# Optimization experiments

Measured on AMD Instinct MI355X. Metric: run time of the kernel, lower is better.

The kernel has to match this reference:

```python
import jax, jax.numpy as jnp
import numpy as np

HEADS = 8
EPS = 1e-5

def _conv2d(x, w, b):
    # x: (b,c,h,w), w: (out_c,in_c,3,3), padding=1 (SAME)
    y = jax.lax.conv_general_dilated(x, w, (1, 1), ((1, 1), (1, 1)),
                                     dimension_numbers=('NCHW', 'OIHW', 'NCHW'))
    return y + b[None, :, None, None]

def _mcl(x, cw, cb, pw):
    # MultichannelLinear: conv then per-channel pointwise matmul over the h (feature) dim
    y = _conv2d(x, cw, cb)                      # (b,c,in_f,w)
    return jnp.einsum('bchw,cfh->bcfw', y, pw)  # (b,c,out_f,w)

def _ln(x, g, b):
    # MultichannelLayerNorm over the feature (h) axis with per-channel affine
    mu = x.mean(axis=2, keepdims=True)
    var = x.var(axis=2, keepdims=True)
    xn = (x - mu) * jax.lax.rsqrt(var + EPS)
    return xn * g[None, :, :, None] + b[None, :, :, None]

def _rope(t):
    # lucidrains RotaryEmbedding.rotate_queries_or_keys, interleaved pairs; t: (...,w,d)
    d = t.shape[-1]
    w = t.shape[-2]
    inv = 1.0 / (10000.0 ** (jnp.arange(0, d, 2, dtype=jnp.float32) / d))
    ang = jnp.arange(w, dtype=jnp.float32)[:, None] * inv[None, :]   # (w, d/2)
    cos = jnp.repeat(jnp.cos(ang), 2, axis=-1)
    sin = jnp.repeat(jnp.sin(ang), 2, axis=-1)
    t2 = t.reshape(t.shape[:-1] + (d // 2, 2))
    rot = jnp.stack([-t2[..., 1], t2[..., 0]], axis=-1).reshape(t.shape)
    return t * cos + rot * sin

def _split_heads(y, nh):
    b, c, f, w = y.shape
    return y.transpose(0, 1, 3, 2).reshape(b, c, w, nh, f // nh).transpose(0, 1, 3, 2, 4)  # (b,c,nh,w,dh)

def _forward(x, embed_cw, embed_cb, embed_pw, norm1_g, norm1_b,
             q_cw, q_cb, q_pw, k_cw, k_cb, k_pw, v_cw, v_cb, v_pw,
             o_cw, o_cb, o_pw, norm2_g, norm2_b,
             ffn1_cw, ffn1_cb, ffn1_pw, ffn2_cw, ffn2_cb, ffn2_pw):
    b, c_in, hdim, w = x.shape
    h0 = _mcl(x, embed_cw, embed_cb, embed_pw)          # (b,c,feat,w)
    # --- multichannel multihead attention with inline RoPE ---
    xn = _ln(h0, norm1_g, norm1_b)
    q = _rope(_split_heads(_mcl(xn, q_cw, q_cb, q_pw), HEADS))   # (b,c,nh,w,dh)
    k = _rope(_split_heads(_mcl(xn, k_cw, k_cb, k_pw), HEADS))
    v = _split_heads(_mcl(xn, v_cw, v_cb, v_pw), HEADS)
    qk = jnp.einsum('bchqd,bchkd->bchqk', q, k) / jnp.sqrt(jnp.float32(hdim))  # scale by sqrt(h), per source
    a = jnp.einsum('bchqk,bchkd->bchqd', jax.nn.softmax(qk, axis=-1), v)
    bb, cc, nh, ww, dh = a.shape
    a = a.transpose(0, 1, 3, 2, 4).reshape(bb, cc, ww, nh * dh).transpose(0, 1, 3, 2)  # (b,c,feat,w)
    z = _mcl(a, o_cw, o_cb, o_pw)
    h = h0 + z
    # --- squared-ReLU FFN ---
    y = _mcl(_ln(h, norm2_g, norm2_b), ffn1_cw, ffn1_cb, ffn1_pw)
    y = jnp.maximum(y, 0.0) ** 2
    z = _mcl(y, ffn2_cw, ffn2_cb, ffn2_pw)
    h = h + z
    return jnp.concatenate([x, h], axis=1)  # (b, c_in+c_out, feat, w)

def setup_inputs() -> dict:
    key = jax.random.key(0)
    ks = jax.random.split(key, 32)
    C_IN, C, F, W, B, EXP = 8, 4, 1024, 512, 4, 4

    def p(k, shape, fan):
        return jax.random.normal(k, shape, dtype=jnp.float32) * (1.0 / np.sqrt(fan))

    inp = {
        'x': jax.random.normal(ks[0], (B, C_IN, F, W), dtype=jnp.float32),
        'embed_cw': p(ks[1], (C, C_IN, 3, 3), C_IN * 9), 'embed_cb': p(ks[2], (C,), C_IN * 9),
        'embed_pw': p(ks[3], (C, F, F), F),
        'norm1_g': jnp.ones((C, F), jnp.float32), 'norm1_b': jnp.zeros((C, F), jnp.float32),
        'q_cw': p(ks[4], (C, C, 3, 3), C * 9), 'q_cb': p(ks[5], (C,), C * 9), 'q_pw': p(ks[6], (C, F, F), F),
        'k_cw': p(ks[7], (C, C, 3, 3), C * 9), 'k_cb': p(ks[8], (C,), C * 9), 'k_pw': p(ks[9], (C, F, F), F),
        'v_cw': p(ks[10], (C, C, 3, 3), C * 9), 'v_cb': p(ks[11], (C,), C * 9), 'v_pw': p(ks[12], (C, F, F), F),
        'o_cw': p(ks[13], (C, C, 3, 3), C * 9), 'o_cb': p(ks[14], (C,), C * 9), 'o_pw': p(ks[15], (C, F, F), F),
        'norm2_g': jnp.ones((C, F), jnp.float32), 'norm2_b': jnp.zeros((C, F), jnp.float32),
        'ffn1_cw': p(ks[16], (C, C, 3, 3), C * 9), 'ffn1_cb': p(ks[17], (C,), C * 9),
        'ffn1_pw': p(ks[18], (C, F * EXP, F), F),
        'ffn2_cw': p(ks[19], (C, C, 3, 3), C * 9), 'ffn2_cb': p(ks[20], (C,), C * 9),
        'ffn2_pw': p(ks[21], (C, F, F * EXP), F * EXP),
    }
    return inp

def reference(x, embed_cw, embed_cb, embed_pw, norm1_g, norm1_b,
              q_cw, q_cb, q_pw, k_cw, k_cb, k_pw, v_cw, v_cb, v_pw,
              o_cw, o_cb, o_pw, norm2_g, norm2_b,
              ffn1_cw, ffn1_cb, ffn1_pw, ffn2_cw, ffn2_cb, ffn2_pw):
    return _forward(x, embed_cw, embed_cb, embed_pw, norm1_g, norm1_b,
                    q_cw, q_cb, q_pw, k_cw, k_cb, k_pw, v_cw, v_cb, v_pw,
                    o_cw, o_cb, o_pw, norm2_g, norm2_b,
                    ffn1_cw, ffn1_cb, ffn1_pw, ffn2_cw, ffn2_cb, ffn2_pw)
```

## Files before the change

### kernel.cpp

```cpp
#include <hip/hip_runtime.h>

typedef __attribute__((ext_vector_type(8))) short short8;
typedef __attribute__((ext_vector_type(4))) float f32x4;
typedef unsigned int uint;
typedef unsigned short ushort;

#define PLF 524288

__device__ __forceinline__ ushort f2bf(float f) {
  uint u = __float_as_uint(f);
  u += 0x7FFF + ((u >> 16) & 1);
  return (ushort)(u >> 16);
}
__device__ __forceinline__ float bf2f(ushort h) {
  return __uint_as_float(((uint)h) << 16);
}
__device__ __forceinline__ int swzf(int r) { return ((r & 3) ^ ((r >> 2) & 3)); }

#define GLOAD16(gp, lp)                                          \
  __builtin_amdgcn_global_load_lds(                              \
      (const __attribute__((address_space(1))) void*)(gp),       \
      (__attribute__((address_space(3))) void*)(lp), 16, 0, 0)

template <int CDT, int BETA, int RELU2, int MFAST, int BCVT, int ROPE>
__global__ __launch_bounds__(256) void mm_kernel(
    const void* __restrict__ Av, const void* __restrict__ Bv, void* __restrict__ Cv,
    int K, int lda, int ldb, int ldc,
    int aDiv, int aMod, long long aS1, long long aS2,
    int bDiv, int bMod, long long bS1, long long bS2,
    int cDiv, int cMod, long long cS1, long long cS2, float alpha)
{
  __shared__ char lds[49152];
  const int nx = gridDim.x, ny = gridDim.y;
  const int nwg = nx * ny * (int)gridDim.z;
  const int o = ((int)blockIdx.z * ny + blockIdx.y) * nx + blockIdx.x;
  const int qd = nwg >> 3, rm = nwg & 7, xcd = o & 7, rot = o >> 3;
  const int wflat = (xcd < rm ? xcd * (qd + 1) : rm * (qd + 1) + (xcd - rm) * qd) + rot;
  int bx, by, bz;
  if (MFAST) { by = wflat % ny; int t2 = wflat / ny; bx = t2 % nx; bz = t2 / nx; }
  else       { bx = wflat % nx; int t2 = wflat / nx; by = t2 % ny; bz = t2 / ny; }
  const int tid = threadIdx.x;
  const long long aOff = (long long)(bz / aDiv) * aS1 + (long long)(bz % aMod) * aS2;
  const long long bOff = (long long)(bz / bDiv) * bS1 + (long long)(bz % bMod) * bS2;
  const long long cOff = (long long)(bz / cDiv) * cS1 + (long long)(bz % cMod) * cS2;
  const int m0 = by * 128, n0 = bx * 128;
  const int lane = tid & 63, wid = tid >> 6;
  const int MOFF = (wid >> 1) * 64, NOFF = (wid & 1) * 64;
  const int u = lane & 15, g = lane >> 4;
  const int sr0 = tid >> 2, sslot = tid & 3;
  const ushort* Ap = (const ushort*)Av + aOff;
  const ushort* Bp = (const ushort*)Bv + bOff;
  const float*  Bf = (const float*)Bv + bOff;

#define STAGE(buf, kt)                                                         \
  {                                                                            \
    _Pragma("unroll")                                                          \
    for (int half = 0; half < 2; ++half) {                                     \
      const int r = sr0 + 64 * half;                                           \
      const int ss = sslot ^ swzf(r);                                          \
      GLOAD16(Ap + (long long)(m0 + r) * lda + (kt) + ss * 8,                  \
              &lds[(buf) * 16384] + wid * 1024 + half * 4096);                 \
      if (BCVT == 0) {                                                         \
        GLOAD16(Bp + (long long)(n0 + r) * ldb + (kt) + ss * 8,                \
                &lds[(buf) * 16384 + 8192] + wid * 1024 + half * 4096);        \
      } else {                                                                 \
        const float* srcB = Bf + (long long)(n0 + r) * ldb + (kt) + ss * 8;    \
        float4 x0 = *(const float4*)srcB;                                      \
        float4 x1 = *(const float4*)(srcB + 4);                                \
        short8 h;                                                              \
        h[0] = (short)f2bf(x0.x); h[1] = (short)f2bf(x0.y);                    \
        h[2] = (short)f2bf(x0.z); h[3] = (short)f2bf(x0.w);                    \
        h[4] = (short)f2bf(x1.x); h[5] = (short)f2bf(x1.y);                    \
        h[6] = (short)f2bf(x1.z); h[7] = (short)f2bf(x1.w);                    \
        *(short8*)(&lds[(buf) * 16384 + 8192] + r * 64 + sslot * 16) = h;      \
      }                                                                        \
    }                                                                          \
  }

  f32x4 acc[4][4];
#pragma unroll
  for (int i = 0; i < 4; ++i)
#pragma unroll
    for (int j = 0; j < 4; ++j) acc[i][j] = (f32x4){0.f, 0.f, 0.f, 0.f};

  const int T = K >> 5;
  STAGE(0, 0);
  if (T > 1) STAGE(1, 32);
  int rb = 0, sb = 2;
  for (int t = 0; t < T; ++t) {
    if (BCVT == 0) {
      if (t + 1 < T) { asm volatile("s_waitcnt vmcnt(4)" ::: "memory"); }
      else           { asm volatile("s_waitcnt vmcnt(0)" ::: "memory"); }
    } else {
      asm volatile("s_waitcnt vmcnt(0) lgkmcnt(0)" ::: "memory");
    }
    __builtin_amdgcn_s_barrier();
    __builtin_amdgcn_sched_barrier(0);
    asm volatile("" ::: "memory");
    if (t + 2 < T) STAGE(sb, (t + 2) * 32);
    const char* Abuf = &lds[rb * 16384];
    const char* Bbuf = &lds[rb * 16384 + 8192];
    short8 af[4], bfr[4];
#pragma unroll
    for (int mi = 0; mi < 4; ++mi) {
      const int r = MOFF + mi * 16 + u;
      af[mi] = *(const short8*)(Abuf + r * 64 + ((g ^ swzf(r)) * 16));
    }
#pragma unroll
    for (int ni = 0; ni < 4; ++ni) {
      const int r = NOFF + ni * 16 + u;
      bfr[ni] = *(const short8*)(Bbuf + r * 64 + ((g ^ swzf(r)) * 16));
    }
#pragma unroll
    for (int mi = 0; mi < 4; ++mi)
#pragma unroll
      for (int ni = 0; ni < 4; ++ni)
        acc[mi][ni] = __builtin_amdgcn_mfma_f32_16x16x32_bf16(af[mi], bfr[ni], acc[mi][ni], 0, 0, 0);
    rb = (rb == 2) ? 0 : rb + 1;
    sb = (sb == 2) ? 0 : sb + 1;
  }
#undef STAGE

#pragma unroll
  for (int mi = 0; mi < 4; ++mi)
#pragma unroll
    for (int ni = 0; ni < 4; ++ni)
#pragma unroll
      for (int q = 0; q < 4; ++q) {
        const int row = m0 + MOFF + mi * 16 + g * 4 + q;
        const int col = n0 + NOFF + ni * 16 + u;
        float v = acc[mi][ni][q] * alpha;
        if (CDT == 0) {
          float* cp = (float*)Cv + cOff + (long long)row * ldc + col;
          if (BETA) v += *cp;
          *cp = v;
        } else {
          if (ROPE) {
            const int j = (col & 127) >> 1;
            const float infr = __expf((float)j * (-9.210340371976184f / 64.f));
            float sn, cs;
            __sincosf((float)row * infr, &sn, &cs);
            const float part = __shfl_xor(v, 1);
            v = (col & 1) ? fmaf(part, sn, v * cs) : fmaf(-part, sn, v * cs);
          }
          if (RELU2) { v = fmaxf(v, 0.f); v = v * v; }
          ((ushort*)Cv)[cOff + (long long)row * ldc + col] = f2bf(v);
        }
      }
}

__global__ __launch_bounds__(256) void fattn_kernel(
    const ushort* __restrict__ Qg, const ushort* __restrict__ Kg,
    const ushort* __restrict__ Vg, ushort* __restrict__ Og)
{
  __shared__ char lds[73728];
  const int hb = blockIdx.y, pl = hb >> 3, h = hb & 7;
  const int q0 = blockIdx.x * 64;
  const int tid = threadIdx.x, lane = tid & 63, wv = tid >> 6;
  const int u = lane & 15, g = lane >> 4;
  const ushort* Qh = Qg + (size_t)pl * PLF + h * 128;
  const ushort* Kh = Kg + (size_t)pl * PLF + h * 128;
  const ushort* Vh = Vg + (size_t)pl * PLF + (size_t)(h * 128) * 512;
  ushort* Oh = Og + (size_t)pl * PLF + h * 128;

  short8 qf[4];
  const int qrow = q0 + wv * 16 + u;
#pragma unroll
  for (int dc = 0; dc < 4; ++dc)
    qf[dc] = *(const short8*)(Qh + (size_t)qrow * 1024 + dc * 32 + g * 8);

#define STAGE_KV(buf, kt)                                                     \
  {                                                                           \
    _Pragma("unroll")                                                         \
    for (int it = 0; it < 4; ++it) {                                          \
      const int off = tid * 16 + it * 4096;                                   \
      const int krow = off >> 8, kslot = (off >> 4) & 15;                     \
      GLOAD16(Kh + (size_t)((kt) * 64 + krow) * 1024 +                        \
                  ((kslot ^ ((krow & 7) << 1)) * 8),                          \
              &lds[(buf) * 16384] + off);                                     \
      const int vrow = off >> 7, vslot = (off >> 4) & 7;                      \
      GLOAD16(Vh + (size_t)vrow * 512 + (kt) * 64 + ((vslot ^ (vrow & 7)) * 8), \
              &lds[32768 + (buf) * 16384] + off);                             \
    }                                                                         \
  }

  f32x4 oacc[8];
#pragma unroll
  for (int i = 0; i < 8; ++i) oacc[i] = (f32x4){0.f, 0.f, 0.f, 0.f};
  float m_run = -3.0e38f, l_run = 0.f;

  STAGE_KV(0, 0);
  asm volatile("s_waitcnt vmcnt(0)" ::: "memory");
  __syncthreads();
  int cur = 0;
  for (int kt = 0; kt < 8; ++kt) {
    if (kt + 1 < 8) STAGE_KV(cur ^ 1, kt + 1);
    f32x4 sacc[4];
#pragma unroll
    for (int kn = 0; kn < 4; ++kn) sacc[kn] = (f32x4){0.f, 0.f, 0.f, 0.f};
#pragma unroll
    for (int kn = 0; kn < 4; ++kn) {
      const int r = kn * 16 + u;
      const char* kb = &lds[cur * 16384] + r * 256;
#pragma unroll
      for (int dc = 0; dc < 4; ++dc) {
        short8 kf = *(const short8*)(kb + (((dc * 4 + g) ^ ((u & 7) << 1)) * 16));
        sacc[kn] = __builtin_amdgcn_mfma_f32_16x16x32_bf16(kf, qf[dc], sacc[kn], 0, 0, 0);
      }
    }
    float pm = -3.0e38f;
#pragma unroll
    for (int kn = 0; kn < 4; ++kn)
#pragma unroll
      for (int r = 0; r < 4; ++r) {
        sacc[kn][r] *= 0.03125f;
        pm = fmaxf(pm, sacc[kn][r]);
      }
    pm = fmaxf(pm, __shfl_xor(pm, 16));
    pm = fmaxf(pm, __shfl_xor(pm, 32));
    const float m_new = fmaxf(m_run, pm);
    const float es = __expf(m_run - m_new);
    float psum = 0.f;
    uint pw[4][2];
#pragma unroll
    for (int kn = 0; kn < 4; ++kn) {
      float p0 = __expf(sacc[kn][0] - m_new);
      float p1 = __expf(sacc[kn][1] - m_new);
      float p2 = __expf(sacc[kn][2] - m_new);
      float p3 = __expf(sacc[kn][3] - m_new);
      psum += (p0 + p1) + (p2 + p3);
      pw[kn][0] = (uint)f2bf(p0) | ((uint)f2bf(p1) << 16);
      pw[kn][1] = (uint)f2bf(p2) | ((uint)f2bf(p3) << 16);
    }
    psum += __shfl_xor(psum, 16);
    psum += __shfl_xor(psum, 32);
    l_run = l_run * es + psum;
    m_run = m_new;
    char* pb = &lds[65536 + wv * 2048] + u * 128 + (g & 1) * 8;
#pragma unroll
    for (int kn = 0; kn < 4; ++kn)
      *(uint2*)(pb + (((2 * kn + (g >> 1)) ^ (u & 7)) * 16)) =
          make_uint2(pw[kn][0], pw[kn][1]);
    float es_o[4];
#pragma unroll
    for (int r = 0; r < 4; ++r) es_o[r] = __shfl(es, g * 4 + r);
#pragma unroll
    for (int nd = 0; nd < 8; ++nd)
#pragma unroll
      for (int r = 0; r < 4; ++r) oacc[nd][r] *= es_o[r];
    const char* prd = &lds[65536 + wv * 2048] + u * 128;
    short8 pf[2];
#pragma unroll
    for (int kc = 0; kc < 2; ++kc)
      pf[kc] = *(const short8*)(prd + (((kc * 4 + g) ^ (u & 7)) * 16));
#pragma unroll
    for (int nd = 0; nd < 8; ++nd) {
      const int vr = nd * 16 + u;
      const char* vb = &lds[32768 + cur * 16384] + vr * 128;
#pragma unroll
      for (int kc = 0; kc < 2; ++kc) {
        short8 vf = *(const short8*)(vb + (((kc * 4 + g) ^ (u & 7)) * 16));
        oacc[nd] = __builtin_amdgcn_mfma_f32_16x16x32_bf16(pf[kc], vf, oacc[nd], 0, 0, 0);
      }
    }
    asm volatile("s_waitcnt vmcnt(0)" ::: "memory");
    __syncthreads();
    cur ^= 1;
  }
#undef STAGE_KV
  const float inv_l = 1.f / l_run;
  float inv_o[4];
#pragma unroll
  for (int r = 0; r < 4; ++r) inv_o[r] = __shfl(inv_l, g * 4 + r);
#pragma unroll
  for (int nd = 0; nd < 8; ++nd)
#pragma unroll
    for (int r = 0; r < 4; ++r) {
      const int row = q0 + wv * 16 + g * 4 + r;
      Oh[(size_t)row * 1024 + nd * 16 + u] = f2bf(oacc[nd][r] * inv_o[r]);
    }
}

__global__ __launch_bounds__(256) void cvt_kernel(
    const float4* __restrict__ s, short8* __restrict__ d)
{
  const int i = blockIdx.x * 256 + threadIdx.x;
  const float4 a = s[2 * i], b = s[2 * i + 1];
  short8 h;
  h[0] = (short)f2bf(a.x); h[1] = (short)f2bf(a.y);
  h[2] = (short)f2bf(a.z); h[3] = (short)f2bf(a.w);
  h[4] = (short)f2bf(b.x); h[5] = (short)f2bf(b.y);
  h[6] = (short)f2bf(b.z); h[7] = (short)f2bf(b.w);
  d[i] = h;
}

template <int CIN>
__global__ __launch_bounds__(256) void conv4c_kernel(
    const ushort* __restrict__ in, const float* __restrict__ wt,
    const float* __restrict__ bias, ushort* __restrict__ outp, int log2F)
{
  const int idx = blockIdx.x * 256 + threadIdx.x;
  const int F8m = (1 << (log2F - 3)) - 1;
  const int f8 = idx & F8m;
  const int w = (idx >> (log2F - 3)) & 511;
  const int bb = idx >> (log2F + 6);
  const int f0 = f8 << 3;
  float acc[4][8];
#pragma unroll
  for (int co = 0; co < 4; ++co) {
    const float bv = bias[co];
#pragma unroll
    for (int j = 0; j < 8; ++j) acc[co][j] = bv;
  }
  const bool lok = f8 > 0, rok = f8 < F8m;
#pragma unroll
  for (int ci = 0; ci < CIN; ++ci) {
    const ushort* base = in + (((size_t)(bb * CIN + ci)) << (log2F + 9));
#pragma unroll
    for (int dxw = 0; dxw < 3; ++dxw) {
      const int w2 = w + dxw - 1;
      if (w2 < 0 || w2 > 511) continue;
      const ushort* rp = base + ((size_t)w2 << log2F) + f0;
      const short8 cen = *(const short8*)rp;
      float xv[10];
      xv[0] = lok ? bf2f(rp[-1]) : 0.f;
#pragma unroll
      for (int j = 0; j < 8; ++j) xv[j + 1] = bf2f((ushort)cen[j]);
      xv[9] = rok ? bf2f(rp[8]) : 0.f;
#pragma unroll
      for (int co = 0; co < 4; ++co) {
        const float* wp = wt + (co * CIN + ci) * 9;
        const float k0 = wp[dxw], k1 = wp[3 + dxw], k2 = wp[6 + dxw];
#pragma unroll
        for (int j = 0; j < 8; ++j)
          acc[co][j] += k0 * xv[j] + k1 * xv[j + 1] + k2 * xv[j + 2];
      }
    }
  }
#pragma unroll
  for (int co = 0; co < 4; ++co) {
    short8 o;
#pragma unroll
    for (int j = 0; j < 8; ++j) o[j] = (short)f2bf(acc[co][j]);
    *(short8*)(outp + (((size_t)(bb * 4 + co)) << (log2F + 9)) + ((size_t)w << log2F) + f0) = o;
  }
}

__global__ __launch_bounds__(256) void conv12c_kernel(
    const ushort* __restrict__ in,
    const float* __restrict__ wq, const float* __restrict__ wk, const float* __restrict__ wv,
    const float* __restrict__ bq, const float* __restrict__ bk, const float* __restrict__ bv,
    ushort* __restrict__ outp, int nPl)
{
  const int idx = blockIdx.x * 256 + threadIdx.x;
  const int f8 = idx & 127;
  const int w = (idx >> 7) & 511;
  const int bb = idx >> 16;
  const int f0 = f8 << 3;
  const float* wsel[3] = {wq, wk, wv};
  float acc[12][8];
#pragma unroll
  for (int co = 0; co < 4; ++co) {
    const float b0 = bq[co], b1 = bk[co], b2 = bv[co];
#pragma unroll
    for (int j = 0; j < 8; ++j) {
      acc[co][j] = b0; acc[4 + co][j] = b1; acc[8 + co][j] = b2;
    }
  }
  const bool lok = f8 > 0, rok = f8 < 127;
#pragma unroll
  for (int ci = 0; ci < 4; ++ci) {
    const ushort* base = in + (((size_t)(bb * 4 + ci)) << 19);
#pragma unroll
    for (int dxw = 0; dxw < 3; ++dxw) {
      const int w2 = w + dxw - 1;
      if (w2 < 0 || w2 > 511) continue;
      const ushort* rp = base + ((size_t)w2 << 10) + f0;
      const short8 cen = *(const short8*)rp;
      float xv[10];
      xv[0] = lok ? bf2f(rp[-1]) : 0.f;
#pragma unroll
      for (int j = 0; j < 8; ++j) xv[j + 1] = bf2f((ushort)cen[j]);
      xv[9] = rok ? bf2f(rp[8]) : 0.f;
#pragma unroll
      for (int pj = 0; pj < 3; ++pj)
#pragma unroll
        for (int co = 0; co < 4; ++co) {
          const float* wp = wsel[pj] + (co * 4 + ci) * 9;
          const float k0 = wp[dxw], k1 = wp[3 + dxw], k2 = wp[6 + dxw];
#pragma unroll
          for (int j = 0; j < 8; ++j)
            acc[pj * 4 + co][j] += k0 * xv[j] + k1 * xv[j + 1] + k2 * xv[j + 2];
        }
    }
  }
#pragma unroll
  for (int pj = 0; pj < 3; ++pj)
#pragma unroll
    for (int co = 0; co < 4; ++co) {
      short8 o;
#pragma unroll
      for (int j = 0; j < 8; ++j) o[j] = (short)f2bf(acc[pj * 4 + co][j]);
      *(short8*)(outp + (((size_t)(pj * nPl + bb * 4 + co)) << 19) +
                 ((size_t)w << 10) + f0) = o;
    }
}

__global__ __launch_bounds__(256) void ln_kernel(
    const float* __restrict__ H, const float* __restrict__ gam,
    const float* __restrict__ bet, ushort* __restrict__ XN)
{
  const int wid = threadIdx.x >> 6, lane = threadIdx.x & 63;
  const int row = blockIdx.x * 4 + wid;
  const int c = (row >> 9) & 3;
  const float* xp = H + (size_t)row * 1024;
  float4 v[4];
  float s = 0.f, q = 0.f;
#pragma unroll
  for (int p = 0; p < 4; ++p) {
    v[p] = *(const float4*)(xp + p * 256 + lane * 4);
    s += v[p].x + v[p].y + v[p].z + v[p].w;
    q += v[p].x * v[p].x + v[p].y * v[p].y + v[p].z * v[p].z + v[p].w * v[p].w;
  }
#pragma unroll
  for (int o = 32; o > 0; o >>= 1) { s += __shfl_xor(s, o); q += __shfl_xor(q, o); }
  const float mu = s * (1.f / 1024.f);
  const float var = q * (1.f / 1024.f) - mu * mu;
  const float rs = rsqrtf(var + 1e-5f);
  ushort* op = XN + (size_t)row * 1024;
  const float* gp = gam + c * 1024;
  const float* bp = bet + c * 1024;
#pragma unroll
  for (int p = 0; p < 4; ++p) {
    const int f = p * 256 + lane * 4;
    float4 g4 = *(const float4*)(gp + f);
    float4 b4 = *(const float4*)(bp + f);
    ushort4 o4;
    o4.x = f2bf((v[p].x - mu) * rs * g4.x + b4.x);
    o4.y = f2bf((v[p].y - mu) * rs * g4.y + b4.y);
    o4.z = f2bf((v[p].z - mu) * rs * g4.z + b4.z);
    o4.w = f2bf((v[p].w - mu) * rs * g4.w + b4.w);
    *(ushort4*)(op + f) = o4;
  }
}

__global__ __launch_bounds__(256) void tin_kernel(
    const float* __restrict__ x, ushort* __restrict__ XT,
    float* __restrict__ outp, int planeOff)
{
  __shared__ float t[32][33];
  const int f0 = blockIdx.x * 32, w0 = blockIdx.y * 32;
  const int z = blockIdx.z;
  const int tx = threadIdx.x & 31, ty = threadIdx.x >> 5;
  const int gpl = planeOff + z;
  const int b = gpl >> 3, ch = gpl & 7;
  const float* src = x + (size_t)gpl * PLF;
  float* dst0 = outp + (size_t)(b * 12 + ch) * PLF;
#pragma unroll
  for (int r = 0; r < 32; r += 8) {
    const size_t off = (size_t)(f0 + r + ty) * 512 + w0 + tx;
    const float v = src[off];
    t[r + ty][tx] = v;
    dst0[off] = v;
  }
  __syncthreads();
  ushort* dst = XT + (size_t)z * PLF;
#pragma unroll
  for (int r = 0; r < 32; r += 8) dst[(size_t)(w0 + r + ty) * 1024 + f0 + tx] = f2bf(t[tx][r + ty]);
}

__global__ __launch_bounds__(256) void tout_kernel(
    const float* __restrict__ H, float* __restrict__ out, int b0)
{
  __shared__ float t[32][33];
  const int w0 = blockIdx.x * 32, f0 = blockIdx.y * 32;
  const int p = blockIdx.z;
  const int b = b0 + (p >> 2), c = p & 3;
  const int tx = threadIdx.x & 31, ty = threadIdx.x >> 5;
  const float* src = H + (size_t)p * PLF;
#pragma unroll
  for (int r = 0; r < 32; r += 8) t[r + ty][tx] = src[(size_t)(w0 + r + ty) * 1024 + f0 + tx];
  __syncthreads();
  float* dst = out + (size_t)(b * 12 + 8 + c) * PLF;
#pragma unroll
  for (int r = 0; r < 32; r += 8) dst[(size_t)(f0 + r + ty) * 512 + w0 + tx] = t[tx][r + ty];
}

extern "C" void kernel_launch(void* const* d_in, const int* in_sizes, int n_in,
                              void* d_out, int out_size, void* d_ws, size_t ws_size,
                              hipStream_t stream)
{
  const float* x        = (const float*)d_in[0];
  const float* embed_cw = (const float*)d_in[1];
  const float* embed_cb = (const float*)d_in[2];
  const float* embed_pw = (const float*)d_in[3];
  const float* n1g      = (const float*)d_in[4];
  const float* n1b      = (const float*)d_in[5];
  const float* q_cw     = (const float*)d_in[6];
  const float* q_cb     = (const float*)d_in[7];
  const float* q_pw     = (const float*)d_in[8];
  const float* k_cw     = (const float*)d_in[9];
  const float* k_cb     = (const float*)d_in[10];
  const float* k_pw     = (const float*)d_in[11];
  const float* v_cw     = (const float*)d_in[12];
  const float* v_cb     = (const float*)d_in[13];
  const float* v_pw     = (const float*)d_in[14];
  const float* o_cw     = (const float*)d_in[15];
  const float* o_cb     = (const float*)d_in[16];
  const float* o_pw     = (const float*)d_in[17];
  const float* n2g      = (const float*)d_in[18];
  const float* n2b      = (const float*)d_in[19];
  const float* f1_cw    = (const float*)d_in[20];
  const float* f1_cb    = (const float*)d_in[21];
  const float* f1_pw    = (const float*)d_in[22];
  const float* f2_cw    = (const float*)d_in[23];
  const float* f2_cb    = (const float*)d_in[24];
  const float* f2_pw    = (const float*)d_in[25];
  float* out = (float*)d_out;

  const size_t perB = 50331648ull;
  const int N = (ws_size >= 4 * perB) ? 4 : (ws_size >= 2 * perB) ? 2 : 1;
  const int nP = 4 * N;

  char* base = (char*)d_ws;
  float*  Hf = (float*)base;
  ushort* XT = (ushort*)(base + (size_t)N * 8388608);
  ushort* XN = (ushort*)((char*)XT + (size_t)N * 8388608);
  ushort* Qb = (ushort*)((char*)XN + (size_t)N * 4194304);
  ushort* Kb = (ushort*)((char*)Qb + (size_t)N * 4194304);
  ushort* CT = (ushort*)((char*)Kb + (size_t)N * 4194304);
  ushort* Vb = (ushort*)((char*)CT + (size_t)N * 4194304);
  ushort* SfPb = (ushort*)((char*)Vb + (size_t)N * 4194304);
  ushort* CT3 = SfPb;
  ushort* W8  = SfPb;
  ushort* WQK = XT;
  ushort* MID = XT;
  ushort* f1w = Vb;
  ushort* F2C = Vb;
  ushort* f2w = XT;

  const long long W1 = 1048576;
  const long long W4 = 4194304;
  const long long M1 = 2097152;
  const long long CH3 = (long long)nP * PLF;
  const int GCc1 = N * 256;
  const int GCc4 = N * 1024;

  for (int b0 = 0; b0 < 4; b0 += N) {
    tin_kernel<<<dim3(32, 16, 8 * N), 256, 0, stream>>>(x, XT, out, b0 * 8);
    conv4c_kernel<8><<<GCc1, 256, 0, stream>>>(XT, embed_cw, embed_cb, CT, 10);
    cvt_kernel<<<2048, 256, 0, stream>>>((const float4*)embed_pw, (short8*)W8);
    mm_kernel<0, 0, 0, 0, 0, 0><<<dim3(8, 4, nP), 256, 0, stream>>>(
        CT, W8, Hf, 1024, 1024, 1024, 1024,
        1, 1, PLF, 0, 4, 4, 0, W1, 1, 1, PLF, 0, 1.f);
    ln_kernel<<<nP * 128, 256, 0, stream>>>(Hf, n1g, n1b, XN);
    conv12c_kernel<<<GCc1, 256, 0, stream>>>(XN, q_cw, k_cw, v_cw,
                                             q_cb, k_cb, v_cb, CT3, nP);
    if (N >= 2) {
      cvt_kernel<<<2048, 256, 0, stream>>>((const float4*)q_pw, (short8*)WQK);
      cvt_kernel<<<2048, 256, 0, stream>>>((const float4*)k_pw, (short8*)(WQK) + 524288);
      mm_kernel<1, 0, 0, 0, 0, 1><<<dim3(8, 4, 2 * nP), 256, 0, stream>>>(
          CT3, WQK, Qb, 1024, 1024, 1024, 1024,
          1, 1, PLF, 0, nP, 4, 4 * W1, W1, 1, 1, PLF, 0, 1.f);
    } else {
      mm_kernel<1, 0, 0, 0, 1, 1><<<dim3(8, 4, nP), 256, 0, stream>>>(
          CT3, q_pw, Qb, 1024, 1024, 1024, 1024,
          1, 1, PLF, 0, 4, 4, 0, W1, 1, 1, PLF, 0, 1.f);
      mm_kernel<1, 0, 0, 0, 1, 1><<<dim3(8, 4, nP), 256, 0, stream>>>(
          CT3 + CH3, k_pw, Kb, 1024, 1024, 1024, 1024,
          1, 1, PLF, 0, 4, 4, 0, W1, 1, 1, PLF, 0, 1.f);
    }
    cvt_kernel<<<2048, 256, 0, stream>>>((const float4*)v_pw, (short8*)W8);
    mm_kernel<1, 0, 0, 0, 0, 0><<<dim3(4, 8, nP), 256, 0, stream>>>(
        W8, CT3 + 2 * CH3, Vb, 1024, 1024, 1024, 512,
        4, 4, 0, W1, 1, 1, PLF, 0, 1, 1, PLF, 0, 1.f);
    fattn_kernel<<<dim3(8, nP * 8), 256, 0, stream>>>(Qb, Kb, Vb, Qb);
    conv4c_kernel<4><<<GCc1, 256, 0, stream>>>(Qb, o_cw, o_cb, CT, 10);
    cvt_kernel<<<2048, 256, 0, stream>>>((const float4*)o_pw, (short8*)W8);
    mm_kernel<0, 1, 0, 0, 0, 0><<<dim3(8, 4, nP), 256, 0, stream>>>(
        CT, W8, Hf, 1024, 1024, 1024, 1024,
        1, 1, PLF, 0, 4, 4, 0, W1, 1, 1, PLF, 0, 1.f);
    ln_kernel<<<nP * 128, 256, 0, stream>>>(Hf, n2g, n2b, XN);
    conv4c_kernel<4><<<GCc1, 256, 0, stream>>>(XN, f1_cw, f1_cb, CT, 10);
    if (N >= 2) {
      cvt_kernel<<<8192, 256, 0, stream>>>((const float4*)f1_pw, (short8*)f1w);
      mm_kernel<1, 0, 1, 1, 0, 0><<<dim3(32, 4, nP), 256, 0, stream>>>(
          CT, f1w, MID, 1024, 1024, 1024, 4096,
          1, 1, PLF, 0, 4, 4, 0, W4, 1, 1, M1, 0, 1.f);
    } else {
      mm_kernel<1, 0, 1, 1, 1, 0><<<dim3(32, 4, nP), 256, 0, stream>>>(
          CT, f1_pw, MID, 1024, 1024, 1024, 4096,
          1, 1, PLF, 0, 4, 4, 0, W4, 1, 1, M1, 0, 1.f);
    }
    conv4c_kernel<4><<<GCc4, 256, 0, stream>>>(MID, f2_cw, f2_cb, F2C, 12);
    if (N >= 2) {
      cvt_kernel<<<8192, 256, 0, stream>>>((const float4*)f2_pw, (short8*)f2w);
      mm_kernel<0, 1, 0, 0, 0, 0><<<dim3(8, 4, nP), 256, 0, stream>>>(
          F2C, f2w, Hf, 4096, 4096, 4096, 1024,
          1, 1, M1, 0, 4, 4, 0, W4, 1, 1, PLF, 0, 1.f);
    } else {
      mm_kernel<0, 1, 0, 0, 1, 0><<<dim3(8, 4, nP), 256, 0, stream>>>(
          F2C, f2_pw, Hf, 4096, 4096, 4096, 1024,
          1, 1, M1, 0, 4, 4, 0, W4, 1, 1, PLF, 0, 1.f);
    }
    tout_kernel<<<dim3(16, 32, nP), 256, 0, stream>>>(Hf, out, b0);
  }
}
```

Before: 651.1 us.

## Compute two output columns per conv thread, add MFMA priority hints, enable MFAST

The 4-output-channel conv kernel now computes two adjacent w positions per thread, so four input rows serve two outputs instead of three rows per output. This cuts redundant input loads and halves the grid. The flash-attention loop raises wave priority around its MFMA blocks with s_setprio, and several matmul launches switch on the MFAST template flag. The conv12c launch gets its own grid-size constant, and per-thread register use in conv4c roughly doubles, which may lower occupancy.

```diff
diff --git a/kernel.cpp b/kernel.cpp
--- a/kernel.cpp
+++ b/kernel.cpp
@@ -198,6 +198,7 @@
     f32x4 sacc[4];
 #pragma unroll
     for (int kn = 0; kn < 4; ++kn) sacc[kn] = (f32x4){0.f, 0.f, 0.f, 0.f};
+    __builtin_amdgcn_s_setprio(1);
 #pragma unroll
     for (int kn = 0; kn < 4; ++kn) {
       const int r = kn * 16 + u;
@@ -208,6 +209,7 @@
         sacc[kn] = __builtin_amdgcn_mfma_f32_16x16x32_bf16(kf, qf[dc], sacc[kn], 0, 0, 0);
       }
     }
+    __builtin_amdgcn_s_setprio(0);
     float pm = -3.0e38f;
 #pragma unroll
     for (int kn = 0; kn < 4; ++kn)
@@ -253,6 +255,7 @@
 #pragma unroll
     for (int kc = 0; kc < 2; ++kc)
       pf[kc] = *(const short8*)(prd + (((kc * 4 + g) ^ (u & 7)) * 16));
+    __builtin_amdgcn_s_setprio(1);
 #pragma unroll
     for (int nd = 0; nd < 8; ++nd) {
       const int vr = nd * 16 + u;
@@ -263,6 +266,7 @@
         oacc[nd] = __builtin_amdgcn_mfma_f32_16x16x32_bf16(pf[kc], vf, oacc[nd], 0, 0, 0);
       }
     }
+    __builtin_amdgcn_s_setprio(0);
     asm volatile("s_waitcnt vmcnt(0)" ::: "memory");
     __syncthreads();
     cur ^= 1;
@@ -302,25 +306,26 @@
   const int idx = blockIdx.x * 256 + threadIdx.x;
   const int F8m = (1 << (log2F - 3)) - 1;
   const int f8 = idx & F8m;
-  const int w = (idx >> (log2F - 3)) & 511;
-  const int bb = idx >> (log2F + 6);
+  const int wp2 = (idx >> (log2F - 3)) & 255;
+  const int bb = idx >> (log2F + 5);
+  const int w = wp2 * 2;
   const int f0 = f8 << 3;
-  float acc[4][8];
+  float acc[2][4][8];
 #pragma unroll
   for (int co = 0; co < 4; ++co) {
     const float bv = bias[co];
 #pragma unroll
-    for (int j = 0; j < 8; ++j) acc[co][j] = bv;
+    for (int j = 0; j < 8; ++j) { acc[0][co][j] = bv; acc[1][co][j] = bv; }
   }
   const bool lok = f8 > 0, rok = f8 < F8m;
 #pragma unroll
   for (int ci = 0; ci < CIN; ++ci) {
     const ushort* base = in + (((size_t)(bb * CIN + ci)) << (log2F + 9));
 #pragma unroll
-    for (int dxw = 0; dxw < 3; ++dxw) {
-      const int w2 = w + dxw - 1;
-      if (w2 < 0 || w2 > 511) continue;
-      const ushort* rp = base + ((size_t)w2 << log2F) + f0;
+    for (int rr = 0; rr < 4; ++rr) {
+      const int wr = w - 1 + rr;
+      if (wr < 0 || wr > 511) continue;
+      const ushort* rp = base + ((size_t)wr << log2F) + f0;
       const short8 cen = *(const short8*)rp;
       float xv[10];
       xv[0] = lok ? bf2f(rp[-1]) : 0.f;
@@ -330,20 +335,31 @@
 #pragma unroll
       for (int co = 0; co < 4; ++co) {
         const float* wp = wt + (co * CIN + ci) * 9;
-        const float k0 = wp[dxw], k1 = wp[3 + dxw], k2 = wp[6 + dxw];
-#pragma unroll
-        for (int j = 0; j < 8; ++j)
-          acc[co][j] += k0 * xv[j] + k1 * xv[j + 1] + k2 * xv[j + 2];
+        if (rr <= 2) {
+          const float k0 = wp[rr], k1 = wp[3 + rr], k2 = wp[6 + rr];
+#pragma unroll
+          for (int j = 0; j < 8; ++j)
+            acc[0][co][j] += k0 * xv[j] + k1 * xv[j + 1] + k2 * xv[j + 2];
+        }
+        if (rr >= 1) {
+          const float k0 = wp[rr - 1], k1 = wp[2 + rr], k2 = wp[5 + rr];
+#pragma unroll
+          for (int j = 0; j < 8; ++j)
+            acc[1][co][j] += k0 * xv[j] + k1 * xv[j + 1] + k2 * xv[j + 2];
+        }
       }
     }
   }
 #pragma unroll
-  for (int co = 0; co < 4; ++co) {
-    short8 o;
-#pragma unroll
-    for (int j = 0; j < 8; ++j) o[j] = (short)f2bf(acc[co][j]);
-    *(short8*)(outp + (((size_t)(bb * 4 + co)) << (log2F + 9)) + ((size_t)w << log2F) + f0) = o;
-  }
+  for (int wo = 0; wo < 2; ++wo)
+#pragma unroll
+    for (int co = 0; co < 4; ++co) {
+      short8 o;
+#pragma unroll
+      for (int j = 0; j < 8; ++j) o[j] = (short)f2bf(acc[wo][co][j]);
+      *(short8*)(outp + (((size_t)(bb * 4 + co)) << (log2F + 9)) +
+                 ((size_t)(w + wo) << log2F) + f0) = o;
+    }
 }
 
 __global__ __launch_bounds__(256) void conv12c_kernel(
@@ -543,30 +559,31 @@
   const long long W4 = 4194304;
   const long long M1 = 2097152;
   const long long CH3 = (long long)nP * PLF;
-  const int GCc1 = N * 256;
-  const int GCc4 = N * 1024;
+  const int GCc1 = N * 128;
+  const int GCc4 = N * 512;
+  const int GC12 = N * 256;
 
   for (int b0 = 0; b0 < 4; b0 += N) {
     tin_kernel<<<dim3(32, 16, 8 * N), 256, 0, stream>>>(x, XT, out, b0 * 8);
     conv4c_kernel<8><<<GCc1, 256, 0, stream>>>(XT, embed_cw, embed_cb, CT, 10);
     cvt_kernel<<<2048, 256, 0, stream>>>((const float4*)embed_pw, (short8*)W8);
-    mm_kernel<0, 0, 0, 0, 0, 0><<<dim3(8, 4, nP), 256, 0, stream>>>(
+    mm_kernel<0, 0, 0, 1, 0, 0><<<dim3(8, 4, nP), 256, 0, stream>>>(
         CT, W8, Hf, 1024, 1024, 1024, 1024,
         1, 1, PLF, 0, 4, 4, 0, W1, 1, 1, PLF, 0, 1.f);
     ln_kernel<<<nP * 128, 256, 0, stream>>>(Hf, n1g, n1b, XN);
-    conv12c_kernel<<<GCc1, 256, 0, stream>>>(XN, q_cw, k_cw, v_cw,
+    conv12c_kernel<<<GC12, 256, 0, stream>>>(XN, q_cw, k_cw, v_cw,
                                              q_cb, k_cb, v_cb, CT3, nP);
     if (N >= 2) {
       cvt_kernel<<<2048, 256, 0, stream>>>((const float4*)q_pw, (short8*)WQK);
       cvt_kernel<<<2048, 256, 0, stream>>>((const float4*)k_pw, (short8*)(WQK) + 524288);
-      mm_kernel<1, 0, 0, 0, 0, 1><<<dim3(8, 4, 2 * nP), 256, 0, stream>>>(
+      mm_kernel<1, 0, 0, 1, 0, 1><<<dim3(8, 4, 2 * nP), 256, 0, stream>>>(
           CT3, WQK, Qb, 1024, 1024, 1024, 1024,
           1, 1, PLF, 0, nP, 4, 4 * W1, W1, 1, 1, PLF, 0, 1.f);
     } else {
-      mm_kernel<1, 0, 0, 0, 1, 1><<<dim3(8, 4, nP), 256, 0, stream>>>(
+      mm_kernel<1, 0, 0, 1, 1, 1><<<dim3(8, 4, nP), 256, 0, stream>>>(
           CT3, q_pw, Qb, 1024, 1024, 1024, 1024,
           1, 1, PLF, 0, 4, 4, 0, W1, 1, 1, PLF, 0, 1.f);
-      mm_kernel<1, 0, 0, 0, 1, 1><<<dim3(8, 4, nP), 256, 0, stream>>>(
+      mm_kernel<1, 0, 0, 1, 1, 1><<<dim3(8, 4, nP), 256, 0, stream>>>(
           CT3 + CH3, k_pw, Kb, 1024, 1024, 1024, 1024,
           1, 1, PLF, 0, 4, 4, 0, W1, 1, 1, PLF, 0, 1.f);
     }
@@ -577,7 +594,7 @@
     fattn_kernel<<<dim3(8, nP * 8), 256, 0, stream>>>(Qb, Kb, Vb, Qb);
     conv4c_kernel<4><<<GCc1, 256, 0, stream>>>(Qb, o_cw, o_cb, CT, 10);
     cvt_kernel<<<2048, 256, 0, stream>>>((const float4*)o_pw, (short8*)W8);
-    mm_kernel<0, 1, 0, 0, 0, 0><<<dim3(8, 4, nP), 256, 0, stream>>>(
+    mm_kernel<0, 1, 0, 1, 0, 0><<<dim3(8, 4, nP), 256, 0, stream>>>(
         CT, W8, Hf, 1024, 1024, 1024, 1024,
         1, 1, PLF, 0, 4, 4, 0, W1, 1, 1, PLF, 0, 1.f);
     ln_kernel<<<nP * 128, 256, 0, stream>>>(Hf, n2g, n2b, XN);
@@ -595,11 +612,11 @@
     conv4c_kernel<4><<<GCc4, 256, 0, stream>>>(MID, f2_cw, f2_cb, F2C, 12);
     if (N >= 2) {
       cvt_kernel<<<8192, 256, 0, stream>>>((const float4*)f2_pw, (short8*)f2w);
-      mm_kernel<0, 1, 0, 0, 0, 0><<<dim3(8, 4, nP), 256, 0, stream>>>(
+      mm_kernel<0, 1, 0, 1, 0, 0><<<dim3(8, 4, nP), 256, 0, stream>>>(
           F2C, f2w, Hf, 4096, 4096, 4096, 1024,
           1, 1, M1, 0, 4, 4, 0, W4, 1, 1, PLF, 0, 1.f);
     } else {
-      mm_kernel<0, 1, 0, 0, 1, 0><<<dim3(8, 4, nP), 256, 0, stream>>>(
+      mm_kernel<0, 1, 0, 1, 1, 0><<<dim3(8, 4, nP), 256, 0, stream>>>(
           F2C, f2_pw, Hf, 4096, 4096, 4096, 1024,
           1, 1, M1, 0, 4, 4, 0, W4, 1, 1, PLF, 0, 1.f);
     }
```

New measurement: 659.7 us. Within noise of the previous version (+1.3%).
